# Kernel optimization log

Hardware: AMD Instinct MI355X
Metric: run time of the kernel (lower is better)

Reference implementation:

```python
import jax, jax.numpy as jnp
import numpy as np

HIDDEN, FFN, N_EXPERTS, TOP_K = 1024, 4096, 8, 2


def setup_inputs() -> dict:
    key = jax.random.key(0)
    ks = jax.random.split(key, 8)
    s_h = 1.0 / np.sqrt(HIDDEN)
    s_f = 1.0 / np.sqrt(FFN)
    return {
        "x": jax.random.normal(ks[0], (1, 1024, HIDDEN), dtype=jnp.float32),
        "gate_w": jax.random.normal(ks[1], (N_EXPERTS, HIDDEN), dtype=jnp.float32) * s_h,
        "gate_b": jnp.zeros((N_EXPERTS,), dtype=jnp.float32),
        "w1": jax.random.normal(ks[2], (N_EXPERTS, HIDDEN, FFN), dtype=jnp.float32) * s_h,
        "b1": jnp.zeros((N_EXPERTS, FFN), dtype=jnp.float32),
        "w2": jax.random.normal(ks[3], (N_EXPERTS, FFN, HIDDEN), dtype=jnp.float32) * s_f,
        "b2": jnp.zeros((N_EXPERTS, HIDDEN), dtype=jnp.float32),
    }


def reference(x, gate_w, gate_b, w1, b1, w2, b2):
    B, S, H = x.shape
    x_flat = x.reshape(-1, H)  # (T, H)
    # Router: top-k gating with softmax over selected logits
    logits = x_flat @ gate_w.T + gate_b  # (T, E)
    top_w, sel = jax.lax.top_k(logits, TOP_K)  # (T, K)
    rw = jax.nn.softmax(top_w, axis=-1)  # (T, K)
    # combine[t, e] = router weight of expert e for token t (0 if not selected)
    combine = jnp.sum(jax.nn.one_hot(sel, N_EXPERTS, dtype=x.dtype) * rw[..., None], axis=1)  # (T, E)
    # Dense all-expert FFN, combined with routing weights (zero weight => zero contribution,
    # identical math to the masked gather/scatter loop in the torch module)
    h = jax.nn.gelu(jnp.einsum('th,ehf->tef', x_flat, w1) + b1, approximate=False)  # (T, E, F)
    y = jnp.einsum('tef,efh->teh', h, w2) + b2  # (T, E, H)
    out = jnp.einsum('te,teh->th', combine, y)  # (T, H)
    return out.reshape(B, S, H)
```

## Files before the change

### kernel.cpp

```cpp
#include <hip/hip_runtime.h>


typedef __bf16 bf16;
typedef __bf16 bf16x8 __attribute__((ext_vector_type(8)));
typedef float floatx4 __attribute__((ext_vector_type(4)));

#define T_TOK 1024
#define HID 1024
#define FFN 4096
#define NEXP 8
#define BM 128
#define BN 128
#define BK 32
#define LP 36

__global__ void xconv_k(const float* __restrict__ x, bf16* __restrict__ xb) {
  int i = blockIdx.x * 256 + threadIdx.x;
  float4 a = ((const float4*)x)[i * 2];
  float4 b = ((const float4*)x)[i * 2 + 1];
  bf16 t[8] = {(bf16)a.x, (bf16)a.y, (bf16)a.z, (bf16)a.w,
               (bf16)b.x, (bf16)b.y, (bf16)b.z, (bf16)b.w};
  *(bf16x8*)&xb[(size_t)i * 8] = *(bf16x8*)t;
}

__global__ void wconv_k(const float* __restrict__ w, bf16* __restrict__ wt,
                        int K, int N, int lgN, int lgKC) {
  int gid = blockIdx.x * 256 + threadIdx.x;
  int n = gid & (N - 1);
  int kc = (gid >> lgN) & ((K >> 5) - 1);
  int e = gid >> (lgN + lgKC);
  const float* src = w + ((size_t)e * K + (size_t)kc * 32) * N + n;
  bf16* dst = wt + ((size_t)e * N + n) * (size_t)K + kc * 32;
  float v[32];
#pragma unroll
  for (int j = 0; j < 32; j++) v[j] = src[(size_t)j * N];
  bf16x8 pk[4];
#pragma unroll
  for (int q = 0; q < 4; q++)
#pragma unroll
    for (int i = 0; i < 8; i++) pk[q][i] = (bf16)v[q * 8 + i];
#pragma unroll
  for (int q = 0; q < 4; q++) *(bf16x8*)(dst + q * 8) = pk[q];
}

__global__ void router_k(const float* __restrict__ x, const float* __restrict__ gw,
                         const float* __restrict__ gb, int* __restrict__ cnt,
                         int* __restrict__ elist, float* __restrict__ ewt) {
  int wave = threadIdx.x >> 6;
  int lane = threadIdx.x & 63;
  int t = blockIdx.x * 4 + wave;
  const float* xr = x + (size_t)t * HID;
  float xv[16];
#pragma unroll
  for (int j = 0; j < 16; j++) xv[j] = xr[lane + 64 * j];
  float logits[NEXP];
#pragma unroll
  for (int e = 0; e < NEXP; e++) {
    const float* g = gw + (size_t)e * HID;
    float s = 0.f;
#pragma unroll
    for (int j = 0; j < 16; j++) s += xv[j] * g[lane + 64 * j];
#pragma unroll
    for (int off = 32; off; off >>= 1) s += __shfl_xor(s, off, 64);
    logits[e] = s + gb[e];
  }
  int i0 = 0; float l0 = logits[0];
#pragma unroll
  for (int e = 1; e < NEXP; e++) if (logits[e] > l0) { l0 = logits[e]; i0 = e; }
  int i1 = -1; float l1 = -3.0e38f;
#pragma unroll
  for (int e = 0; e < NEXP; e++) if (e != i0 && logits[e] > l1) { l1 = logits[e]; i1 = e; }
  if (lane == 0) {
    float w0 = 1.f / (1.f + expf(l1 - l0));
    float w1 = 1.f - w0;
    int p0 = atomicAdd(cnt + i0, 1);
    elist[i0 * T_TOK + p0] = t * 2 + 0; ewt[i0 * T_TOK + p0] = w0;
    int p1 = atomicAdd(cnt + i1, 1);
    elist[i1 * T_TOK + p1] = t * 2 + 1; ewt[i1 * T_TOK + p1] = w1;
  }
}

__global__ __launch_bounds__(256)
void gemm1_k(const bf16* __restrict__ xb, const bf16* __restrict__ w1t,
             const float* __restrict__ b1, const int* __restrict__ cnt,
             const int* __restrict__ elist, bf16* __restrict__ hbuf) {
  int e = blockIdx.z;
  int c = cnt[e];
  int m0 = blockIdx.y * BM;
  if (m0 >= c) return;
  int n0 = blockIdx.x * BN;

  __shared__ __align__(16) bf16 As[BM][LP];
  __shared__ __align__(16) bf16 Bs[BN][LP];

  int tid = threadIdx.x;
  int ar = tid >> 1;
  int ac = (tid & 1) * 16;
  int ra = m0 + ar; if (ra >= c) ra = c - 1;
  const bf16* aptr = xb + (size_t)(elist[e * T_TOK + ra] >> 1) * HID + ac;
  const bf16* bptr = w1t + (size_t)e * FFN * HID + (size_t)(n0 + ar) * HID + ac;

  uint4 a0, a1, b0, b1r;
  a0 = *(const uint4*)(aptr);
  a1 = *(const uint4*)(aptr + 8);
  b0 = *(const uint4*)(bptr);
  b1r = *(const uint4*)(bptr + 8);

  floatx4 acc[4][4] = {};
  int ln = tid & 63, wv = tid >> 6;
  int fm = ln & 15, quad = ln >> 4;
  int wm = (wv & 1) * 64, wn = (wv >> 1) * 64;

  for (int t = 0; t < HID / BK; t++) {
    uint4 wa0 = a0, wa1 = a1, wb0 = b0, wb1 = b1r;
    __syncthreads();
    *(uint4*)&As[ar][ac]     = wa0;
    *(uint4*)&As[ar][ac + 8] = wa1;
    *(uint4*)&Bs[ar][ac]     = wb0;
    *(uint4*)&Bs[ar][ac + 8] = wb1;
    if (t + 1 < HID / BK) {
      aptr += BK;
      bptr += BK;
      a0 = *(const uint4*)(aptr);
      a1 = *(const uint4*)(aptr + 8);
      b0 = *(const uint4*)(bptr);
      b1r = *(const uint4*)(bptr + 8);
    }
    __syncthreads();
    bf16x8 af[4], bfr[4];
#pragma unroll
    for (int i = 0; i < 4; i++) af[i] = *(const bf16x8*)&As[wm + i * 16 + fm][quad * 8];
#pragma unroll
    for (int j = 0; j < 4; j++) bfr[j] = *(const bf16x8*)&Bs[wn + j * 16 + fm][quad * 8];
#pragma unroll
    for (int i = 0; i < 4; i++)
#pragma unroll
      for (int j = 0; j < 4; j++)
        acc[i][j] = __builtin_amdgcn_mfma_f32_16x16x32_bf16(af[i], bfr[j], acc[i][j], 0, 0, 0);
  }

  const float* b1e = b1 + (size_t)e * FFN;
#pragma unroll
  for (int i = 0; i < 4; i++) {
    int rb = m0 + wm + i * 16 + quad * 4;
#pragma unroll
    for (int j = 0; j < 4; j++) {
      int col = n0 + wn + j * 16 + fm;
      float bias = b1e[col];
#pragma unroll
      for (int r = 0; r < 4; r++) {
        int row = rb + r;
        if (row < c) {
          int slot = elist[e * T_TOK + row];
          float v = acc[i][j][r] + bias;
          float g = 0.5f * v * (1.f + erff(v * 0.70710678118654752f));
          hbuf[(size_t)slot * FFN + col] = (bf16)g;
        }
      }
    }
  }
}

__global__ __launch_bounds__(256)
void gemm2_k(const bf16* __restrict__ hbuf, const bf16* __restrict__ w2t,
             const float* __restrict__ b2, const int* __restrict__ cnt,
             const int* __restrict__ elist, const float* __restrict__ ewt,
             float* __restrict__ part) {
  int e = blockIdx.z & 7;
  int ks = blockIdx.z >> 3;
  int c = cnt[e];
  int m0 = blockIdx.y * BM;
  if (m0 >= c) return;
  int n0 = blockIdx.x * BN;
  int kbeg = ks * (FFN / 4);

  __shared__ __align__(16) bf16 As[BM][LP];
  __shared__ __align__(16) bf16 Bs[BN][LP];

  int tid = threadIdx.x;
  int ar = tid >> 1;
  int ac = (tid & 1) * 16;
  int ra = m0 + ar; if (ra >= c) ra = c - 1;
  const bf16* aptr = hbuf + (size_t)elist[e * T_TOK + ra] * FFN + kbeg + ac;
  const bf16* bptr = w2t + (size_t)e * HID * FFN + (size_t)(n0 + ar) * FFN + kbeg + ac;

  uint4 a0, a1, b0, b1r;
  a0 = *(const uint4*)(aptr);
  a1 = *(const uint4*)(aptr + 8);
  b0 = *(const uint4*)(bptr);
  b1r = *(const uint4*)(bptr + 8);

  floatx4 acc[4][4] = {};
  int ln = tid & 63, wv = tid >> 6;
  int fm = ln & 15, quad = ln >> 4;
  int wm = (wv & 1) * 64, wn = (wv >> 1) * 64;

  const int NT = (FFN / 4) / BK;
  for (int t = 0; t < NT; t++) {
    uint4 wa0 = a0, wa1 = a1, wb0 = b0, wb1 = b1r;
    __syncthreads();
    *(uint4*)&As[ar][ac]     = wa0;
    *(uint4*)&As[ar][ac + 8] = wa1;
    *(uint4*)&Bs[ar][ac]     = wb0;
    *(uint4*)&Bs[ar][ac + 8] = wb1;
    if (t + 1 < NT) {
      aptr += BK;
      bptr += BK;
      a0 = *(const uint4*)(aptr);
      a1 = *(const uint4*)(aptr + 8);
      b0 = *(const uint4*)(bptr);
      b1r = *(const uint4*)(bptr + 8);
    }
    __syncthreads();
    bf16x8 af[4], bfr[4];
#pragma unroll
    for (int i = 0; i < 4; i++) af[i] = *(const bf16x8*)&As[wm + i * 16 + fm][quad * 8];
#pragma unroll
    for (int j = 0; j < 4; j++) bfr[j] = *(const bf16x8*)&Bs[wn + j * 16 + fm][quad * 8];
#pragma unroll
    for (int i = 0; i < 4; i++)
#pragma unroll
      for (int j = 0; j < 4; j++)
        acc[i][j] = __builtin_amdgcn_mfma_f32_16x16x32_bf16(af[i], bfr[j], acc[i][j], 0, 0, 0);
  }

  const float* b2e = b2 + (size_t)e * HID;
#pragma unroll
  for (int i = 0; i < 4; i++) {
    int rb = m0 + wm + i * 16 + quad * 4;
#pragma unroll
    for (int j = 0; j < 4; j++) {
      int col = n0 + wn + j * 16 + fm;
      float bias = (ks == 0) ? b2e[col] : 0.f;
#pragma unroll
      for (int r = 0; r < 4; r++) {
        int row = rb + r;
        if (row < c) {
          int slot = elist[e * T_TOK + row];
          float w = ewt[e * T_TOK + row];
          part[((size_t)ks * (2 * T_TOK) + slot) * HID + col] = w * (acc[i][j][r] + bias);
        }
      }
    }
  }
}

__global__ void combine_k(const float* __restrict__ part, float* __restrict__ out) {
  int i = blockIdx.x * 256 + threadIdx.x;
  int t = i >> 8;
  int h4 = (i & 255) * 4;
  float4 s = {0.f, 0.f, 0.f, 0.f};
#pragma unroll
  for (int ks = 0; ks < 4; ks++)
#pragma unroll
    for (int sl = 0; sl < 2; sl++) {
      float4 v = *(const float4*)&part[((size_t)ks * (2 * T_TOK) + t * 2 + sl) * HID + h4];
      s.x += v.x; s.y += v.y; s.z += v.z; s.w += v.w;
    }
  *(float4*)&out[(size_t)t * HID + h4] = s;
}

extern "C" void kernel_launch(void* const* d_in, const int* in_sizes, int n_in,
                              void* d_out, int out_size, void* d_ws, size_t ws_size,
                              hipStream_t stream) {
  const float* x  = (const float*)d_in[0];
  const float* gw = (const float*)d_in[1];
  const float* gb = (const float*)d_in[2];
  const float* w1 = (const float*)d_in[3];
  const float* b1 = (const float*)d_in[4];
  const float* w2 = (const float*)d_in[5];
  const float* b2 = (const float*)d_in[6];
  float* out = (float*)d_out;

  char* ws = (char*)d_ws;
  int*   cnt   = (int*)ws;
  int*   elist = (int*)(ws + 1024);
  float* ewt   = (float*)(ws + 1024 + 32768);
  bf16*  xb    = (bf16*)(ws + (1 << 16));
  bf16*  hbuf  = (bf16*)(ws + ((size_t)4 << 20));
  float* part  = (float*)(ws + ((size_t)21 << 20));
  bf16*  wT    = (bf16*)(ws + ((size_t)55 << 20));

  hipMemsetAsync(cnt, 0, 32, stream);
  xconv_k<<<512, 256, 0, stream>>>(x, xb);
  router_k<<<T_TOK / 4, 256, 0, stream>>>(x, gw, gb, cnt, elist, ewt);
  wconv_k<<<4096, 256, 0, stream>>>(w1, wT, HID, FFN, 12, 5);
  gemm1_k<<<dim3(FFN / BN, 8, NEXP), 256, 0, stream>>>(xb, wT, b1, cnt, elist, hbuf);
  wconv_k<<<4096, 256, 0, stream>>>(w2, wT, FFN, HID, 10, 7);
  gemm2_k<<<dim3(HID / BN, 8, NEXP * 4), 256, 0, stream>>>(hbuf, wT, b2, cnt, elist, ewt, part);
  combine_k<<<(T_TOK * HID / 4) / 256, 256, 0, stream>>>(part, out);
}
```

Baseline: 481.8 us.

## Fuse conversion/router launches, use direct global-to-LDS loads, atomically combine outputs

Merges the x conversion, router and w1 conversion into one launch, and runs the w2 conversion inside the gemm1 grid when the workspace is large enough, so independent work overlaps. Both GEMMs now stage tiles with global_load_lds straight into unpadded LDS instead of register prefetch plus padded stores. The combine kernel and partial buffer are dropped in favour of float atomicAdd into a zeroed output. Costs: the register double-buffer prefetch is lost, unpadded LDS may cause bank conflicts, and atomics make the summation order nondeterministic.

```diff
diff --git a/kernel.cpp b/kernel.cpp
--- a/kernel.cpp
+++ b/kernel.cpp
@@ -12,20 +12,15 @@
 #define BM 128
 #define BN 128
 #define BK 32
-#define LP 36
-
-__global__ void xconv_k(const float* __restrict__ x, bf16* __restrict__ xb) {
-  int i = blockIdx.x * 256 + threadIdx.x;
-  float4 a = ((const float4*)x)[i * 2];
-  float4 b = ((const float4*)x)[i * 2 + 1];
-  bf16 t[8] = {(bf16)a.x, (bf16)a.y, (bf16)a.z, (bf16)a.w,
-               (bf16)b.x, (bf16)b.y, (bf16)b.z, (bf16)b.w};
-  *(bf16x8*)&xb[(size_t)i * 8] = *(bf16x8*)t;
-}
-
-__global__ void wconv_k(const float* __restrict__ w, bf16* __restrict__ wt,
-                        int K, int N, int lgN, int lgKC) {
-  int gid = blockIdx.x * 256 + threadIdx.x;
+
+#define GLOAD16(g, l) __builtin_amdgcn_global_load_lds( \
+    (const __attribute__((address_space(1))) void*)(g), \
+    (__attribute__((address_space(3))) void*)(l), 16, 0, 0)
+
+__device__ __forceinline__ void wconv_body(const float* __restrict__ w,
+                                           bf16* __restrict__ wt, int bid, int tid,
+                                           int K, int N, int lgN, int lgKC) {
+  int gid = bid * 256 + tid;
   int n = gid & (N - 1);
   int kc = (gid >> lgN) & ((K >> 5) - 1);
   int e = gid >> (lgN + lgKC);
@@ -43,12 +38,24 @@
   for (int q = 0; q < 4; q++) *(bf16x8*)(dst + q * 8) = pk[q];
 }
 
-__global__ void router_k(const float* __restrict__ x, const float* __restrict__ gw,
-                         const float* __restrict__ gb, int* __restrict__ cnt,
-                         int* __restrict__ elist, float* __restrict__ ewt) {
-  int wave = threadIdx.x >> 6;
-  int lane = threadIdx.x & 63;
-  int t = blockIdx.x * 4 + wave;
+__device__ __forceinline__ void xconv_body(const float* __restrict__ x,
+                                           bf16* __restrict__ xb, int bid, int tid) {
+  int i = bid * 256 + tid;
+  float4 a = ((const float4*)x)[i * 2];
+  float4 b = ((const float4*)x)[i * 2 + 1];
+  bf16 t[8] = {(bf16)a.x, (bf16)a.y, (bf16)a.z, (bf16)a.w,
+               (bf16)b.x, (bf16)b.y, (bf16)b.z, (bf16)b.w};
+  *(bf16x8*)&xb[(size_t)i * 8] = *(bf16x8*)t;
+}
+
+__device__ __forceinline__ void router_body(const float* __restrict__ x,
+                                            const float* __restrict__ gw,
+                                            const float* __restrict__ gb,
+                                            int* __restrict__ cnt, int* __restrict__ elist,
+                                            float* __restrict__ ewt, int bid, int tid) {
+  int wave = tid >> 6;
+  int lane = tid & 63;
+  int t = bid * 4 + wave;
   const float* xr = x + (size_t)t * HID;
   float xv[16];
 #pragma unroll
@@ -81,51 +88,65 @@
 }
 
 __global__ __launch_bounds__(256)
-void gemm1_k(const bf16* __restrict__ xb, const bf16* __restrict__ w1t,
-             const float* __restrict__ b1, const int* __restrict__ cnt,
-             const int* __restrict__ elist, bf16* __restrict__ hbuf) {
-  int e = blockIdx.z;
+void fusedB_k(const float* __restrict__ x, bf16* __restrict__ xb,
+              const float* __restrict__ gw, const float* __restrict__ gb,
+              int* __restrict__ cnt, int* __restrict__ elist, float* __restrict__ ewt,
+              const float* __restrict__ w1, bf16* __restrict__ w1t) {
+  int bid = blockIdx.x;
+  int tid = threadIdx.x;
+  if (bid < 4096) { wconv_body(w1, w1t, bid, tid, HID, FFN, 12, 5); return; }
+  bid -= 4096;
+  if (bid < 512) { xconv_body(x, xb, bid, tid); return; }
+  router_body(x, gw, gb, cnt, elist, ewt, bid - 512, tid);
+}
+
+__global__ __launch_bounds__(256)
+void wconv_k(const float* __restrict__ w, bf16* __restrict__ wt,
+             int K, int N, int lgN, int lgKC) {
+  wconv_body(w, wt, blockIdx.x, threadIdx.x, K, N, lgN, lgKC);
+}
+
+__global__ __launch_bounds__(256)
+void gemm1f_k(int nconv, const float* __restrict__ w2, bf16* __restrict__ w2t,
+              const bf16* __restrict__ xb, const bf16* __restrict__ w1t,
+              const float* __restrict__ b1, const int* __restrict__ cnt,
+              const int* __restrict__ elist, bf16* __restrict__ hbuf) {
+  int tid = threadIdx.x;
+  int bid = blockIdx.x;
+  if (bid < nconv) { wconv_body(w2, w2t, bid, tid, FFN, HID, 10, 7); return; }
+  int g = bid - nconv;
+  int e = g >> 8;
+  int m0 = ((g >> 5) & 7) * BM;
+  int n0 = (g & 31) * BN;
   int c = cnt[e];
-  int m0 = blockIdx.y * BM;
   if (m0 >= c) return;
-  int n0 = blockIdx.x * BN;
-
-  __shared__ __align__(16) bf16 As[BM][LP];
-  __shared__ __align__(16) bf16 Bs[BN][LP];
-
-  int tid = threadIdx.x;
-  int ar = tid >> 1;
-  int ac = (tid & 1) * 16;
-  int ra = m0 + ar; if (ra >= c) ra = c - 1;
-  const bf16* aptr = xb + (size_t)(elist[e * T_TOK + ra] >> 1) * HID + ac;
-  const bf16* bptr = w1t + (size_t)e * FFN * HID + (size_t)(n0 + ar) * HID + ac;
-
-  uint4 a0, a1, b0, b1r;
-  a0 = *(const uint4*)(aptr);
-  a1 = *(const uint4*)(aptr + 8);
-  b0 = *(const uint4*)(bptr);
-  b1r = *(const uint4*)(bptr + 8);
+
+  __shared__ __align__(16) bf16 As[BM][BK];
+  __shared__ __align__(16) bf16 Bs[BN][BK];
+
+  int l = tid & 63, w = tid >> 6;
+  int rr = w * 32 + (l >> 2);
+  int cb = (l & 3) * 8;
+  int ga0 = m0 + rr;      if (ga0 >= c) ga0 = c - 1;
+  int ga1 = m0 + rr + 16; if (ga1 >= c) ga1 = c - 1;
+  const bf16* aS0 = xb + (size_t)(elist[e * T_TOK + ga0] >> 1) * HID + cb;
+  const bf16* aS1 = xb + (size_t)(elist[e * T_TOK + ga1] >> 1) * HID + cb;
+  const bf16* w1te = w1t + (size_t)e * FFN * HID;
+  const bf16* bS0 = w1te + (size_t)(n0 + rr) * HID + cb;
+  const bf16* bS1 = w1te + (size_t)(n0 + rr + 16) * HID + cb;
+  bf16* ldA0 = &As[w * 32][0];
+  bf16* ldA1 = &As[w * 32 + 16][0];
+  bf16* ldB0 = &Bs[w * 32][0];
+  bf16* ldB1 = &Bs[w * 32 + 16][0];
 
   floatx4 acc[4][4] = {};
-  int ln = tid & 63, wv = tid >> 6;
-  int fm = ln & 15, quad = ln >> 4;
-  int wm = (wv & 1) * 64, wn = (wv >> 1) * 64;
+  int fm = l & 15, quad = l >> 4, wm = (w & 1) * 64, wn = (w >> 1) * 64;
 
   for (int t = 0; t < HID / BK; t++) {
-    uint4 wa0 = a0, wa1 = a1, wb0 = b0, wb1 = b1r;
-    __syncthreads();
-    *(uint4*)&As[ar][ac]     = wa0;
-    *(uint4*)&As[ar][ac + 8] = wa1;
-    *(uint4*)&Bs[ar][ac]     = wb0;
-    *(uint4*)&Bs[ar][ac + 8] = wb1;
-    if (t + 1 < HID / BK) {
-      aptr += BK;
-      bptr += BK;
-      a0 = *(const uint4*)(aptr);
-      a1 = *(const uint4*)(aptr + 8);
-      b0 = *(const uint4*)(bptr);
-      b1r = *(const uint4*)(bptr + 8);
-    }
+    __syncthreads();
+    GLOAD16(aS0, ldA0); GLOAD16(aS1, ldA1);
+    GLOAD16(bS0, ldB0); GLOAD16(bS1, ldB1);
+    aS0 += BK; aS1 += BK; bS0 += BK; bS1 += BK;
     __syncthreads();
     bf16x8 af[4], bfr[4];
 #pragma unroll
@@ -153,8 +174,8 @@
         if (row < c) {
           int slot = elist[e * T_TOK + row];
           float v = acc[i][j][r] + bias;
-          float g = 0.5f * v * (1.f + erff(v * 0.70710678118654752f));
-          hbuf[(size_t)slot * FFN + col] = (bf16)g;
+          float gl = 0.5f * v * (1.f + erff(v * 0.70710678118654752f));
+          hbuf[(size_t)slot * FFN + col] = (bf16)gl;
         }
       }
     }
@@ -165,7 +186,7 @@
 void gemm2_k(const bf16* __restrict__ hbuf, const bf16* __restrict__ w2t,
              const float* __restrict__ b2, const int* __restrict__ cnt,
              const int* __restrict__ elist, const float* __restrict__ ewt,
-             float* __restrict__ part) {
+             float* __restrict__ out) {
   int e = blockIdx.z & 7;
   int ks = blockIdx.z >> 3;
   int c = cnt[e];
@@ -174,43 +195,34 @@
   int n0 = blockIdx.x * BN;
   int kbeg = ks * (FFN / 4);
 
-  __shared__ __align__(16) bf16 As[BM][LP];
-  __shared__ __align__(16) bf16 Bs[BN][LP];
+  __shared__ __align__(16) bf16 As[BM][BK];
+  __shared__ __align__(16) bf16 Bs[BN][BK];
 
   int tid = threadIdx.x;
-  int ar = tid >> 1;
-  int ac = (tid & 1) * 16;
-  int ra = m0 + ar; if (ra >= c) ra = c - 1;
-  const bf16* aptr = hbuf + (size_t)elist[e * T_TOK + ra] * FFN + kbeg + ac;
-  const bf16* bptr = w2t + (size_t)e * HID * FFN + (size_t)(n0 + ar) * FFN + kbeg + ac;
-
-  uint4 a0, a1, b0, b1r;
-  a0 = *(const uint4*)(aptr);
-  a1 = *(const uint4*)(aptr + 8);
-  b0 = *(const uint4*)(bptr);
-  b1r = *(const uint4*)(bptr + 8);
+  int l = tid & 63, w = tid >> 6;
+  int rr = w * 32 + (l >> 2);
+  int cb = (l & 3) * 8;
+  int ga0 = m0 + rr;      if (ga0 >= c) ga0 = c - 1;
+  int ga1 = m0 + rr + 16; if (ga1 >= c) ga1 = c - 1;
+  const bf16* aS0 = hbuf + (size_t)elist[e * T_TOK + ga0] * FFN + kbeg + cb;
+  const bf16* aS1 = hbuf + (size_t)elist[e * T_TOK + ga1] * FFN + kbeg + cb;
+  const bf16* w2te = w2t + (size_t)e * HID * FFN;
+  const bf16* bS0 = w2te + (size_t)(n0 + rr) * FFN + kbeg + cb;
+  const bf16* bS1 = w2te + (size_t)(n0 + rr + 16) * FFN + kbeg + cb;
+  bf16* ldA0 = &As[w * 32][0];
+  bf16* ldA1 = &As[w * 32 + 16][0];
+  bf16* ldB0 = &Bs[w * 32][0];
+  bf16* ldB1 = &Bs[w * 32 + 16][0];
 
   floatx4 acc[4][4] = {};
-  int ln = tid & 63, wv = tid >> 6;
-  int fm = ln & 15, quad = ln >> 4;
-  int wm = (wv & 1) * 64, wn = (wv >> 1) * 64;
+  int fm = l & 15, quad = l >> 4, wm = (w & 1) * 64, wn = (w >> 1) * 64;
 
   const int NT = (FFN / 4) / BK;
   for (int t = 0; t < NT; t++) {
-    uint4 wa0 = a0, wa1 = a1, wb0 = b0, wb1 = b1r;
-    __syncthreads();
-    *(uint4*)&As[ar][ac]     = wa0;
-    *(uint4*)&As[ar][ac + 8] = wa1;
-    *(uint4*)&Bs[ar][ac]     = wb0;
-    *(uint4*)&Bs[ar][ac + 8] = wb1;
-    if (t + 1 < NT) {
-      aptr += BK;
-      bptr += BK;
-      a0 = *(const uint4*)(aptr);
-      a1 = *(const uint4*)(aptr + 8);
-      b0 = *(const uint4*)(bptr);
-      b1r = *(const uint4*)(bptr + 8);
-    }
+    __syncthreads();
+    GLOAD16(aS0, ldA0); GLOAD16(aS1, ldA1);
+    GLOAD16(bS0, ldB0); GLOAD16(bS1, ldB1);
+    aS0 += BK; aS1 += BK; bS0 += BK; bS1 += BK;
     __syncthreads();
     bf16x8 af[4], bfr[4];
 #pragma unroll
@@ -237,27 +249,12 @@
         int row = rb + r;
         if (row < c) {
           int slot = elist[e * T_TOK + row];
-          float w = ewt[e * T_TOK + row];
-          part[((size_t)ks * (2 * T_TOK) + slot) * HID + col] = w * (acc[i][j][r] + bias);
+          float wgt = ewt[e * T_TOK + row];
+          atomicAdd(&out[(size_t)(slot >> 1) * HID + col], wgt * (acc[i][j][r] + bias));
         }
       }
     }
   }
-}
-
-__global__ void combine_k(const float* __restrict__ part, float* __restrict__ out) {
-  int i = blockIdx.x * 256 + threadIdx.x;
-  int t = i >> 8;
-  int h4 = (i & 255) * 4;
-  float4 s = {0.f, 0.f, 0.f, 0.f};
-#pragma unroll
-  for (int ks = 0; ks < 4; ks++)
-#pragma unroll
-    for (int sl = 0; sl < 2; sl++) {
-      float4 v = *(const float4*)&part[((size_t)ks * (2 * T_TOK) + t * 2 + sl) * HID + h4];
-      s.x += v.x; s.y += v.y; s.z += v.z; s.w += v.w;
-    }
-  *(float4*)&out[(size_t)t * HID + h4] = s;
 }
 
 extern "C" void kernel_launch(void* const* d_in, const int* in_sizes, int n_in,
@@ -278,15 +275,19 @@
   float* ewt   = (float*)(ws + 1024 + 32768);
   bf16*  xb    = (bf16*)(ws + (1 << 16));
   bf16*  hbuf  = (bf16*)(ws + ((size_t)4 << 20));
-  float* part  = (float*)(ws + ((size_t)21 << 20));
-  bf16*  wT    = (bf16*)(ws + ((size_t)55 << 20));
+  bf16*  w1T   = (bf16*)(ws + ((size_t)21 << 20));
+  bool par = ws_size >= ((size_t)157 << 20);
+  bf16*  w2T   = par ? (bf16*)(ws + ((size_t)89 << 20))
+                     : w1T;
 
   hipMemsetAsync(cnt, 0, 32, stream);
-  xconv_k<<<512, 256, 0, stream>>>(x, xb);
-  router_k<<<T_TOK / 4, 256, 0, stream>>>(x, gw, gb, cnt, elist, ewt);
-  wconv_k<<<4096, 256, 0, stream>>>(w1, wT, HID, FFN, 12, 5);
-  gemm1_k<<<dim3(FFN / BN, 8, NEXP), 256, 0, stream>>>(xb, wT, b1, cnt, elist, hbuf);
-  wconv_k<<<4096, 256, 0, stream>>>(w2, wT, FFN, HID, 10, 7);
-  gemm2_k<<<dim3(HID / BN, 8, NEXP * 4), 256, 0, stream>>>(hbuf, wT, b2, cnt, elist, ewt, part);
-  combine_k<<<(T_TOK * HID / 4) / 256, 256, 0, stream>>>(part, out);
-}
+  hipMemsetAsync(out, 0, out_size, stream);
+  fusedB_k<<<4864, 256, 0, stream>>>(x, xb, gw, gb, cnt, elist, ewt, w1, w1T);
+  if (par) {
+    gemm1f_k<<<4096 + 2048, 256, 0, stream>>>(4096, w2, w2T, xb, w1T, b1, cnt, elist, hbuf);
+  } else {
+    gemm1f_k<<<2048, 256, 0, stream>>>(0, w2, w2T, xb, w1T, b1, cnt, elist, hbuf);
+    wconv_k<<<4096, 256, 0, stream>>>(w2, w2T, FFN, HID, 10, 7);
+  }
+  gemm2_k<<<dim3(HID / BN, T_TOK / BM, NEXP * 4), 256, 0, stream>>>(hbuf, w2T, b2, cnt, elist, ewt, out);
+}
```

Measured after the change: 524.6 us. +8.9%, slower.
